# Kernel optimization log

Hardware: AMD Instinct MI355X
Metric: run time of the kernel (lower is better)

Reference implementation:

```python
import jax, jax.numpy as jnp
import numpy as np

B, S, F, H, C, L = 256, 128, 128, 512, 64, 16


def setup_inputs() -> dict:
    key = jax.random.key(0)
    ks = jax.random.split(key, 16)
    stdv = 1.0 / np.sqrt(H)
    u = lambda k, shape, s=stdv: jax.random.uniform(k, shape, jnp.float32, -s, s)
    W_ih = u(ks[0], (F, 4 * H))
    b_ih = u(ks[1], (4 * H,)).at[H:2 * H].set(1.0)  # forget-gate bias init = 1
    W_hh = u(ks[2], (H, 4 * H))
    b_hh = u(ks[3], (4 * H,)).at[H:2 * H].set(1.0)
    cg_w1 = u(ks[4], (C, H))
    cg_b1 = u(ks[5], (H,))
    cg_w2 = u(ks[6], (H, 3 * H))
    cg_b2 = jnp.ones((3 * H,), jnp.float32)  # context_gate[-2].bias.fill_(1.0)
    mu_w = u(ks[7], (H, L))
    mu_b = u(ks[8], (L,))
    lv_w = u(ks[9], (H, L))
    lv_b = u(ks[10], (L,))
    dec_w1 = u(ks[11], (L, H))
    dec_b1 = u(ks[12], (H,))
    dec_w2 = u(ks[13], (H, F))
    dec_b2 = u(ks[14], (F,))
    kx, kc, ke = jax.random.split(ks[15], 3)
    return dict(
        x=jax.random.normal(kx, (B, S, F), jnp.float32),
        context=jax.random.normal(kc, (B, C), jnp.float32),
        eps=jax.random.normal(ke, (B, L), jnp.float32),
        W_ih=W_ih, b_ih=b_ih, W_hh=W_hh, b_hh=b_hh,
        cg_w1=cg_w1, cg_b1=cg_b1, cg_w2=cg_w2, cg_b2=cg_b2,
        mu_w=mu_w, mu_b=mu_b, lv_w=lv_w, lv_b=lv_b,
        dec_w1=dec_w1, dec_b1=dec_b1, dec_w2=dec_w2, dec_b2=dec_b2,
    )


def reference(x, context, eps, W_ih, b_ih, W_hh, b_hh, cg_w1, cg_b1, cg_w2, cg_b2,
              mu_w, mu_b, lv_w, lv_b, dec_w1, dec_b1, dec_w2, dec_b2):
    Bsz, Slen, _ = x.shape
    Hd = W_hh.shape[0]
    # context is static across time -> context-gate computed once (same math as
    # recomputing identically at each step)
    ctx = jax.nn.sigmoid(jax.nn.relu(context @ cg_w1 + cg_b1) @ cg_w2 + cg_b2)  # [B, 3H]
    ci, cf, co = jnp.split(ctx, 3, axis=1)
    # precompute input projections for all timesteps: [S, B, 4H]
    xg = jnp.einsum('bsf,fk->sbk', x, W_ih) + b_ih

    def step(carry, xg_t):
        h, c = carry
        gates = xg_t + h @ W_hh + b_hh
        i, f, g, o = jnp.split(gates, 4, axis=1)
        i = jax.nn.sigmoid(i) * ci
        f = jax.nn.sigmoid(f) * cf
        g = jnp.tanh(g)
        o = jax.nn.sigmoid(o) * co
        c_next = f * c + i * g
        h_next = o * jnp.tanh(c_next)
        return (h_next, c_next), None

    h0 = jnp.zeros((Bsz, Hd), x.dtype)
    (h, _), _ = jax.lax.scan(step, (h0, h0), xg)

    mu = h @ mu_w + mu_b
    log_var = h @ lv_w + lv_b
    z = mu + eps * jnp.exp(0.5 * log_var)  # reparameterize
    recon_x = jax.nn.relu(z @ dec_w1 + dec_b1) @ dec_w2 + dec_b2
    return recon_x, mu, log_var
```

## Files before the change

### kernel.cpp

```cpp
#include <hip/hip_runtime.h>
#include <cstdint>
#include <cstddef>

#define B_ 256
#define S_ 128
#define F_ 128
#define H_ 512
#define C_ 64
#define L_ 16

typedef __attribute__((ext_vector_type(8))) short short8;
typedef __attribute__((ext_vector_type(4))) float f4;
typedef __attribute__((ext_vector_type(4))) unsigned int u4;

__device__ __forceinline__ unsigned short f2bf(float f) {
  union { float f; unsigned u; } v; v.f = f;
  unsigned r = v.u + 0x7fffu + ((v.u >> 16) & 1u);
  return (unsigned short)(r >> 16);
}
__device__ __forceinline__ float sigmoid_(float x) { return 1.0f / (1.0f + __expf(-x)); }
__device__ __forceinline__ float tanh_(float x) {
  x = fminf(15.f, fmaxf(-15.f, x));
  float e = __expf(2.f * x);
  return (e - 1.f) / (e + 1.f);
}

__global__ void fused_pre(const float* __restrict__ W_hh, const float* __restrict__ W_ih,
                          const float* __restrict__ b_ih, const float* __restrict__ b_hh,
                          const float* __restrict__ x, const float* __restrict__ context,
                          const float* __restrict__ cg_w1, const float* __restrict__ cg_b1,
                          unsigned short* __restrict__ Wpk, unsigned short* __restrict__ Wipk,
                          float* __restrict__ bc, unsigned short* __restrict__ xfr,
                          float* __restrict__ hid1) {
  int bid = blockIdx.x;
  if (bid < 648) {
    int t = bid * blockDim.x + threadIdx.x;
    if (t < 131072) {
      int lane = t & 63, r = t >> 6;
      int kit = r & 15, z = r >> 4;
      int gate = z & 3, w = (z >> 2) & 3, g = z >> 4;
      int col = gate * 512 + g * 64 + w * 16 + (lane & 15);
      int k0 = kit * 32 + ((lane >> 4) << 3);
#pragma unroll
      for (int j = 0; j < 8; j++)
        Wpk[t * 8 + j] = f2bf(W_hh[(k0 + j) * 2048 + col]);
    } else if (t < 131072 + 32768) {
      int t2 = t - 131072;
      int lane = t2 & 63, r = t2 >> 6;
      int kit = r & 3, z = r >> 2;
      int gate = z & 3, w = (z >> 2) & 3, g = z >> 4;
      int col = gate * 512 + g * 64 + w * 16 + (lane & 15);
      int k0 = kit * 32 + ((lane >> 4) << 3);
#pragma unroll
      for (int j = 0; j < 8; j++)
        Wipk[t2 * 8 + j] = f2bf(W_ih[(k0 + j) * 2048 + col]);
    } else if (t < 131072 + 32768 + 2048) {
      int i = t - 131072 - 32768;
      bc[i] = b_ih[i] + b_hh[i];
    }
  } else if (bid < 2696) {
    int o8 = (bid - 648) * blockDim.x + threadIdx.x;
    int m = o8 & 15, kb = (o8 >> 4) & 15, Rg = (o8 >> 8) & 15, s = o8 >> 12;
    int b = Rg * 16 + m;
    const float* src = x + (b * S_ + s) * F_ + kb * 8;
    unsigned short* dst = xfr + o8 * 8;
#pragma unroll
    for (int j = 0; j < 8; j++) dst[j] = f2bf(src[j]);
  } else {
    __shared__ float cc[C_];
    int b = bid - 2696, t = threadIdx.x;
    if (t < C_) cc[t] = context[b * C_ + t];
    __syncthreads();
    for (int j = t; j < H_; j += 256) {
      float acc = cg_b1[j];
#pragma unroll 8
      for (int k = 0; k < C_; k++) acc = fmaf(cc[k], cg_w1[k * H_ + j], acc);
      hid1[b * H_ + j] = fmaxf(acc, 0.f);
    }
  }
}

__global__ void ctx2_kernel(const float* __restrict__ hid1, const float* __restrict__ w2,
                            const float* __restrict__ b2, float* __restrict__ ctxg) {
  __shared__ float hr[4 * H_];
  int r0 = blockIdx.x * 4, t = threadIdx.x;
  for (int i = t; i < 4 * H_; i += 256) hr[i] = hid1[r0 * H_ + i];
  __syncthreads();
  float acc[4][6];
#pragma unroll
  for (int r = 0; r < 4; r++)
#pragma unroll
    for (int i = 0; i < 6; i++) acc[r][i] = 0.f;
  for (int k = 0; k < H_; k++) {
    float w[6];
#pragma unroll
    for (int i = 0; i < 6; i++) w[i] = w2[k * 1536 + t + i * 256];
#pragma unroll
    for (int r = 0; r < 4; r++) {
      float hv = hr[r * H_ + k];
#pragma unroll
      for (int i = 0; i < 6; i++) acc[r][i] = fmaf(hv, w[i], acc[r][i]);
    }
  }
#pragma unroll
  for (int r = 0; r < 4; r++)
#pragma unroll
    for (int i = 0; i < 6; i++) {
      int col = t + i * 256;
      ctxg[(r0 + r) * 1536 + col] = sigmoid_(acc[r][i] + b2[col]);
    }
}

__global__ void __launch_bounds__(256, 1) lstm_kernel(
    const unsigned short* __restrict__ xfr, const unsigned short* __restrict__ Wpk,
    const unsigned short* __restrict__ Wipk, const float* __restrict__ bc,
    const float* __restrict__ ctxg, float* __restrict__ hfinal,
    unsigned int* __restrict__ hb0, unsigned int* __restrict__ hb1) {
  __shared__ __align__(16) unsigned short lds_h[8192];

  int tid = threadIdx.x, lane = tid & 63, wid = tid >> 6;
  int bt = blockIdx.x >> 3, g = blockIdx.x & 7;

  short8 wf[4][16], wfi[4][4];
#pragma unroll
  for (int gate = 0; gate < 4; gate++) {
    const short8* wp = (const short8*)Wpk + (size_t)((g * 16 + wid * 4 + gate) * 16) * 64 + lane;
#pragma unroll
    for (int kit = 0; kit < 16; kit++) wf[gate][kit] = wp[kit * 64];
    const short8* wip = (const short8*)Wipk + (size_t)((g * 16 + wid * 4 + gate) * 4) * 64 + lane;
#pragma unroll
    for (int kit = 0; kit < 4; kit++) wfi[gate][kit] = wip[kit * 64];
  }

  int q = lane >> 4, n = lane & 15;
  int colglob = g * 64 + wid * 16 + n;
  float ci_[4], cf_[4], co_[4], cst[4] = {0.f, 0.f, 0.f, 0.f};
#pragma unroll
  for (int r = 0; r < 4; r++) {
    int brow = bt * 16 + q * 4 + r;
    ci_[r] = ctxg[brow * 1536 + colglob];
    cf_[r] = ctxg[brow * 1536 + 512 + colglob];
    co_[r] = ctxg[brow * 1536 + 1024 + colglob];
  }
  float bi = bc[colglob], bff = bc[512 + colglob], bgg = bc[1024 + colglob], bo = bc[1536 + colglob];

  int hsub = (bt * 16 + (colglob >> 5)) * 512 + ((colglob >> 3) & 3) * 128 + (colglob & 7);

  for (int t = 0; t < S_; t++) {
    const unsigned int* hread = (t & 1) ? hb1 : hb0;
    unsigned int* hwrite = (t & 1) ? hb0 : hb1;
    unsigned tt = (unsigned)t;
    unsigned tt1 = (unsigned)(t + 1);

    u4 xt[4];
#pragma unroll
    for (int kit = 0; kit < 4; kit++)
      xt[kit] = *(const u4*)(xfr + ((size_t)(t * 16 + bt) * 4 + kit) * 512 + lane * 8);

    u4 a0, a1, a2, a3, a4, a5, a6, a7;
    {
      const unsigned int* base = hread + (bt * 16 + wid * 4) * 512 + lane * 8;
      const unsigned int* p0 = base;
      const unsigned int* p1 = base + 4;
      const unsigned int* p2 = base + 512;
      const unsigned int* p3 = base + 516;
      const unsigned int* p4 = base + 1024;
      const unsigned int* p5 = base + 1028;
      const unsigned int* p6 = base + 1536;
      const unsigned int* p7 = base + 1540;
      for (;;) {
        asm volatile(
            "global_load_dwordx4 %0, %8, off sc0 sc1\n\t"
            "global_load_dwordx4 %1, %9, off sc0 sc1\n\t"
            "global_load_dwordx4 %2, %10, off sc0 sc1\n\t"
            "global_load_dwordx4 %3, %11, off sc0 sc1\n\t"
            "global_load_dwordx4 %4, %12, off sc0 sc1\n\t"
            "global_load_dwordx4 %5, %13, off sc0 sc1\n\t"
            "global_load_dwordx4 %6, %14, off sc0 sc1\n\t"
            "global_load_dwordx4 %7, %15, off sc0 sc1\n\t"
            "s_waitcnt vmcnt(0)"
            : "=&v"(a0), "=&v"(a1), "=&v"(a2), "=&v"(a3),
              "=&v"(a4), "=&v"(a5), "=&v"(a6), "=&v"(a7)
            : "v"(p0), "v"(p1), "v"(p2), "v"(p3),
              "v"(p4), "v"(p5), "v"(p6), "v"(p7)
            : "memory");
        unsigned bad = 0;
#pragma unroll
        for (int c = 0; c < 4; c++) {
          bad |= (a0[c] >> 16) ^ tt; bad |= (a1[c] >> 16) ^ tt;
          bad |= (a2[c] >> 16) ^ tt; bad |= (a3[c] >> 16) ^ tt;
          bad |= (a4[c] >> 16) ^ tt; bad |= (a5[c] >> 16) ^ tt;
          bad |= (a6[c] >> 16) ^ tt; bad |= (a7[c] >> 16) ^ tt;
        }
        if (__all(bad == 0)) break;
      }
    }

    {
      u4 P;
      P.x = (a0[0] & 0xffffu) | (a0[1] << 16);
      P.y = (a0[2] & 0xffffu) | (a0[3] << 16);
      P.z = (a1[0] & 0xffffu) | (a1[1] << 16);
      P.w = (a1[2] & 0xffffu) | (a1[3] << 16);
      *(u4*)(lds_h + (wid * 4 + 0) * 512 + lane * 8) = P;
      P.x = (a2[0] & 0xffffu) | (a2[1] << 16);
      P.y = (a2[2] & 0xffffu) | (a2[3] << 16);
      P.z = (a3[0] & 0xffffu) | (a3[1] << 16);
      P.w = (a3[2] & 0xffffu) | (a3[3] << 16);
      *(u4*)(lds_h + (wid * 4 + 1) * 512 + lane * 8) = P;
      P.x = (a4[0] & 0xffffu) | (a4[1] << 16);
      P.y = (a4[2] & 0xffffu) | (a4[3] << 16);
      P.z = (a5[0] & 0xffffu) | (a5[1] << 16);
      P.w = (a5[2] & 0xffffu) | (a5[3] << 16);
      *(u4*)(lds_h + (wid * 4 + 2) * 512 + lane * 8) = P;
      P.x = (a6[0] & 0xffffu) | (a6[1] << 16);
      P.y = (a6[2] & 0xffffu) | (a6[3] << 16);
      P.z = (a7[0] & 0xffffu) | (a7[1] << 16);
      P.w = (a7[2] & 0xffffu) | (a7[3] << 16);
      *(u4*)(lds_h + (wid * 4 + 3) * 512 + lane * 8) = P;
    }
    __syncthreads();

    f4 acc[4];
#pragma unroll
    for (int gate = 0; gate < 4; gate++) acc[gate] = (f4){0.f, 0.f, 0.f, 0.f};
#pragma unroll
    for (int kit = 0; kit < 4; kit++) {
      short8 a = __builtin_bit_cast(short8, xt[kit]);
#pragma unroll
      for (int gate = 0; gate < 4; gate++)
        acc[gate] = __builtin_amdgcn_mfma_f32_16x16x32_bf16(a, wfi[gate][kit], acc[gate], 0, 0, 0);
    }

#pragma unroll
    for (int kit = 0; kit < 16; kit++) {
      short8 a = *(const short8*)(lds_h + kit * 512 + lane * 8);
#pragma unroll
      for (int gate = 0; gate < 4; gate++)
        acc[gate] = __builtin_amdgcn_mfma_f32_16x16x32_bf16(a, wf[gate][kit], acc[gate], 0, 0, 0);
    }

    float hv[4];
#pragma unroll
    for (int r = 0; r < 4; r++) {
      float gi = acc[0][r] + bi, gf = acc[1][r] + bff, gc = acc[2][r] + bgg, go = acc[3][r] + bo;
      float iv = ci_[r] * sigmoid_(gi);
      float fv = cf_[r] * sigmoid_(gf);
      float ov = co_[r] * sigmoid_(go);
      float gv = tanh_(gc);
      float c = fv * cst[r] + iv * gv;
      cst[r] = c;
      hv[r] = ov * tanh_(c);
    }

#pragma unroll
    for (int r = 0; r < 4; r++) {
      unsigned int* d = hwrite + hsub + (q * 4 + r) * 8;
      unsigned val = (tt1 << 16) | (unsigned)f2bf(hv[r]);
      asm volatile("global_store_dword %0, %1, off sc0 sc1" :: "v"(d), "v"(val) : "memory");
    }
    if (t == S_ - 1) {
#pragma unroll
      for (int r = 0; r < 4; r++)
        hfinal[(bt * 16 + q * 4 + r) * H_ + colglob] = hv[r];
    }
    __syncthreads();
  }
}

__global__ void post_kernel(const float* __restrict__ hfinal, const float* __restrict__ eps,
                            const float* __restrict__ mu_w, const float* __restrict__ mu_b,
                            const float* __restrict__ lv_w, const float* __restrict__ lv_b,
                            const float* __restrict__ dw1, const float* __restrict__ db1,
                            const float* __restrict__ dw2, const float* __restrict__ db2,
                            float* __restrict__ out) {
  __shared__ float sh[H_], sh1[H_], smu[L_], slv[L_], sz[L_];
  int b = blockIdx.x, t = threadIdx.x;
  for (int i = t; i < H_; i += 256) sh[i] = hfinal[b * H_ + i];
  __syncthreads();
  {
    int o = t >> 3, sub = t & 7, l = o & 15;
    const float* w = (o < 16) ? mu_w : lv_w;
    float acc = 0.f;
    int k0 = sub * 64;
#pragma unroll 8
    for (int k = k0; k < k0 + 64; k++) acc = fmaf(sh[k], w[k * L_ + l], acc);
#pragma unroll
    for (int d = 4; d >= 1; d >>= 1) acc += __shfl_down(acc, d, 8);
    if (sub == 0) {
      if (o < 16) { float v = acc + mu_b[l]; smu[l] = v; out[32768 + b * 16 + l] = v; }
      else        { float v = acc + lv_b[l]; slv[l] = v; out[36864 + b * 16 + l] = v; }
    }
  }
  __syncthreads();
  if (t < L_) sz[t] = smu[t] + eps[b * L_ + t] * __expf(0.5f * slv[t]);
  __syncthreads();
  for (int j = t; j < H_; j += 256) {
    float acc = db1[j];
#pragma unroll
    for (int l = 0; l < L_; l++) acc = fmaf(sz[l], dw1[l * H_ + j], acc);
    sh1[j] = fmaxf(acc, 0.f);
  }
  __syncthreads();
  if (t < F_) {
    float acc = db2[t];
    for (int k = 0; k < H_; k++) acc = fmaf(sh1[k], dw2[k * F_ + t], acc);
    out[b * F_ + t] = acc;
  }
}

extern "C" void kernel_launch(void* const* d_in, const int* in_sizes, int n_in,
                              void* d_out, int out_size, void* d_ws, size_t ws_size,
                              hipStream_t stream) {
  const float* x      = (const float*)d_in[0];
  const float* ctxin  = (const float*)d_in[1];
  const float* eps    = (const float*)d_in[2];
  const float* W_ih   = (const float*)d_in[3];
  const float* b_ih   = (const float*)d_in[4];
  const float* W_hh   = (const float*)d_in[5];
  const float* b_hh   = (const float*)d_in[6];
  const float* cg_w1  = (const float*)d_in[7];
  const float* cg_b1  = (const float*)d_in[8];
  const float* cg_w2  = (const float*)d_in[9];
  const float* cg_b2  = (const float*)d_in[10];
  const float* mu_w   = (const float*)d_in[11];
  const float* mu_b   = (const float*)d_in[12];
  const float* lv_w   = (const float*)d_in[13];
  const float* lv_b   = (const float*)d_in[14];
  const float* dec_w1 = (const float*)d_in[15];
  const float* dec_b1 = (const float*)d_in[16];
  const float* dec_w2 = (const float*)d_in[17];
  const float* dec_b2 = (const float*)d_in[18];
  float* out = (float*)d_out;

  char* ws = (char*)d_ws;
  size_t off = 0;
  auto alloc = [&](size_t bytes) { char* p = ws + off; off = (off + bytes + 255) & ~(size_t)255; return p; };

  unsigned int* hb0 = (unsigned int*)alloc((size_t)B_ * H_ * 4);
  unsigned int* hb1 = (unsigned int*)alloc((size_t)B_ * H_ * 4);
  size_t zero_bytes = off;
  unsigned short* xfr  = (unsigned short*)alloc((size_t)B_ * S_ * F_ * 2);
  unsigned short* Wpk  = (unsigned short*)alloc((size_t)H_ * 2048 * 2);
  unsigned short* Wipk = (unsigned short*)alloc((size_t)F_ * 2048 * 2);
  float* bc    = (float*)alloc(2048 * 4);
  float* ctxg  = (float*)alloc((size_t)B_ * 1536 * 4);
  float* hid1  = (float*)alloc((size_t)B_ * H_ * 4);
  float* hfin  = (float*)alloc((size_t)B_ * H_ * 4);
  (void)ws_size; (void)in_sizes; (void)n_in; (void)out_size;

  hipMemsetAsync(d_ws, 0, zero_bytes, stream);

  fused_pre<<<2952, 256, 0, stream>>>(W_hh, W_ih, b_ih, b_hh, x, ctxin, cg_w1, cg_b1,
                                      Wpk, Wipk, bc, xfr, hid1);
  ctx2_kernel<<<64, 256, 0, stream>>>(hid1, cg_w2, cg_b2, ctxg);
  lstm_kernel<<<128, 256, 0, stream>>>(xfr, Wpk, Wipk, bc, ctxg, hfin, hb0, hb1);
  post_kernel<<<256, 256, 0, stream>>>(hfin, eps, mu_w, mu_b, lv_w, lv_b,
                                       dec_w1, dec_b1, dec_w2, dec_b2, out);
}
```

Baseline: 650.4 us.

## Double-buffer LDS hidden state, drop trailing barrier, selectively re-poll stale loads

The LDS buffer holding the hidden state becomes double-buffered per timestep, which lets the trailing __syncthreads at the end of each step be removed. The spin-wait on the cross-block hidden-state flags now reloads only the chunks that are still stale, with an s_sleep between polls, instead of reissuing all eight loads. Sigmoid and tanh use the hardware reciprocal instead of a full-precision division, while the context-gate sigmoid keeps exact division. Together these target per-step synchronisation and polling overhead in the sequential recurrence, at the cost of slightly lower activation precision and possible added latency from the sleep.

```diff
diff --git a/kernel.cpp b/kernel.cpp
--- a/kernel.cpp
+++ b/kernel.cpp
@@ -18,11 +18,13 @@
   unsigned r = v.u + 0x7fffu + ((v.u >> 16) & 1u);
   return (unsigned short)(r >> 16);
 }
-__device__ __forceinline__ float sigmoid_(float x) { return 1.0f / (1.0f + __expf(-x)); }
+__device__ __forceinline__ float sigmoid_(float x) {
+  return __builtin_amdgcn_rcpf(1.0f + __expf(-x));
+}
 __device__ __forceinline__ float tanh_(float x) {
   x = fminf(15.f, fmaxf(-15.f, x));
   float e = __expf(2.f * x);
-  return (e - 1.f) / (e + 1.f);
+  return (e - 1.f) * __builtin_amdgcn_rcpf(e + 1.f);
 }
 
 __global__ void fused_pre(const float* __restrict__ W_hh, const float* __restrict__ W_ih,
@@ -107,7 +109,7 @@
 #pragma unroll
     for (int i = 0; i < 6; i++) {
       int col = t + i * 256;
-      ctxg[(r0 + r) * 1536 + col] = sigmoid_(acc[r][i] + b2[col]);
+      ctxg[(r0 + r) * 1536 + col] = 1.0f / (1.0f + __expf(-(acc[r][i] + b2[col])));
     }
 }
 
@@ -116,7 +118,7 @@
     const unsigned short* __restrict__ Wipk, const float* __restrict__ bc,
     const float* __restrict__ ctxg, float* __restrict__ hfinal,
     unsigned int* __restrict__ hb0, unsigned int* __restrict__ hb1) {
-  __shared__ __align__(16) unsigned short lds_h[8192];
+  __shared__ __align__(16) unsigned short lds_h[2][8192];
 
   int tid = threadIdx.x, lane = tid & 63, wid = tid >> 6;
   int bt = blockIdx.x >> 3, g = blockIdx.x & 7;
@@ -149,6 +151,7 @@
   for (int t = 0; t < S_; t++) {
     const unsigned int* hread = (t & 1) ? hb1 : hb0;
     unsigned int* hwrite = (t & 1) ? hb0 : hb1;
+    int cur = t & 1;
     unsigned tt = (unsigned)t;
     unsigned tt1 = (unsigned)(t + 1);
 
@@ -168,56 +171,108 @@
       const unsigned int* p5 = base + 1028;
       const unsigned int* p6 = base + 1536;
       const unsigned int* p7 = base + 1540;
-      for (;;) {
+      asm volatile(
+          "global_load_dwordx4 %0, %8, off sc0 sc1\n\t"
+          "global_load_dwordx4 %1, %9, off sc0 sc1\n\t"
+          "global_load_dwordx4 %2, %10, off sc0 sc1\n\t"
+          "global_load_dwordx4 %3, %11, off sc0 sc1\n\t"
+          "global_load_dwordx4 %4, %12, off sc0 sc1\n\t"
+          "global_load_dwordx4 %5, %13, off sc0 sc1\n\t"
+          "global_load_dwordx4 %6, %14, off sc0 sc1\n\t"
+          "global_load_dwordx4 %7, %15, off sc0 sc1\n\t"
+          "s_waitcnt vmcnt(0)"
+          : "=&v"(a0), "=&v"(a1), "=&v"(a2), "=&v"(a3),
+            "=&v"(a4), "=&v"(a5), "=&v"(a6), "=&v"(a7)
+          : "v"(p0), "v"(p1), "v"(p2), "v"(p3),
+            "v"(p4), "v"(p5), "v"(p6), "v"(p7)
+          : "memory");
+      auto bad = [&](const u4& a) -> unsigned {
+        return ((a[0] >> 16) ^ tt) | ((a[1] >> 16) ^ tt)
+             | ((a[2] >> 16) ^ tt) | ((a[3] >> 16) ^ tt);
+      };
+      unsigned m = (__any((int)(bad(a0) != 0)) ? 1u : 0u)
+                 | (__any((int)(bad(a1) != 0)) ? 2u : 0u)
+                 | (__any((int)(bad(a2) != 0)) ? 4u : 0u)
+                 | (__any((int)(bad(a3) != 0)) ? 8u : 0u)
+                 | (__any((int)(bad(a4) != 0)) ? 16u : 0u)
+                 | (__any((int)(bad(a5) != 0)) ? 32u : 0u)
+                 | (__any((int)(bad(a6) != 0)) ? 64u : 0u)
+                 | (__any((int)(bad(a7) != 0)) ? 128u : 0u);
+      while (m) {
+        __builtin_amdgcn_s_sleep(2);
         asm volatile(
-            "global_load_dwordx4 %0, %8, off sc0 sc1\n\t"
-            "global_load_dwordx4 %1, %9, off sc0 sc1\n\t"
-            "global_load_dwordx4 %2, %10, off sc0 sc1\n\t"
-            "global_load_dwordx4 %3, %11, off sc0 sc1\n\t"
-            "global_load_dwordx4 %4, %12, off sc0 sc1\n\t"
-            "global_load_dwordx4 %5, %13, off sc0 sc1\n\t"
-            "global_load_dwordx4 %6, %14, off sc0 sc1\n\t"
-            "global_load_dwordx4 %7, %15, off sc0 sc1\n\t"
+            "s_bitcmp1_b32 %16, 0\n\t"
+            "s_cbranch_scc0 Lp0_%=\n\t"
+            "global_load_dwordx4 %0, %8, off sc0 sc1\n"
+            "Lp0_%=:\n\t"
+            "s_bitcmp1_b32 %16, 1\n\t"
+            "s_cbranch_scc0 Lp1_%=\n\t"
+            "global_load_dwordx4 %1, %9, off sc0 sc1\n"
+            "Lp1_%=:\n\t"
+            "s_bitcmp1_b32 %16, 2\n\t"
+            "s_cbranch_scc0 Lp2_%=\n\t"
+            "global_load_dwordx4 %2, %10, off sc0 sc1\n"
+            "Lp2_%=:\n\t"
+            "s_bitcmp1_b32 %16, 3\n\t"
+            "s_cbranch_scc0 Lp3_%=\n\t"
+            "global_load_dwordx4 %3, %11, off sc0 sc1\n"
+            "Lp3_%=:\n\t"
+            "s_bitcmp1_b32 %16, 4\n\t"
+            "s_cbranch_scc0 Lp4_%=\n\t"
+            "global_load_dwordx4 %4, %12, off sc0 sc1\n"
+            "Lp4_%=:\n\t"
+            "s_bitcmp1_b32 %16, 5\n\t"
+            "s_cbranch_scc0 Lp5_%=\n\t"
+            "global_load_dwordx4 %5, %13, off sc0 sc1\n"
+            "Lp5_%=:\n\t"
+            "s_bitcmp1_b32 %16, 6\n\t"
+            "s_cbranch_scc0 Lp6_%=\n\t"
+            "global_load_dwordx4 %6, %14, off sc0 sc1\n"
+            "Lp6_%=:\n\t"
+            "s_bitcmp1_b32 %16, 7\n\t"
+            "s_cbranch_scc0 Lp7_%=\n\t"
+            "global_load_dwordx4 %7, %15, off sc0 sc1\n"
+            "Lp7_%=:\n\t"
             "s_waitcnt vmcnt(0)"
-            : "=&v"(a0), "=&v"(a1), "=&v"(a2), "=&v"(a3),
-              "=&v"(a4), "=&v"(a5), "=&v"(a6), "=&v"(a7)
+            : "+v"(a0), "+v"(a1), "+v"(a2), "+v"(a3),
+              "+v"(a4), "+v"(a5), "+v"(a6), "+v"(a7)
             : "v"(p0), "v"(p1), "v"(p2), "v"(p3),
-              "v"(p4), "v"(p5), "v"(p6), "v"(p7)
-            : "memory");
-        unsigned bad = 0;
-#pragma unroll
-        for (int c = 0; c < 4; c++) {
-          bad |= (a0[c] >> 16) ^ tt; bad |= (a1[c] >> 16) ^ tt;
-          bad |= (a2[c] >> 16) ^ tt; bad |= (a3[c] >> 16) ^ tt;
-          bad |= (a4[c] >> 16) ^ tt; bad |= (a5[c] >> 16) ^ tt;
-          bad |= (a6[c] >> 16) ^ tt; bad |= (a7[c] >> 16) ^ tt;
-        }
-        if (__all(bad == 0)) break;
+              "v"(p4), "v"(p5), "v"(p6), "v"(p7), "s"(m)
+            : "memory", "scc");
+        m = (__any((int)(bad(a0) != 0)) ? 1u : 0u)
+          | (__any((int)(bad(a1) != 0)) ? 2u : 0u)
+          | (__any((int)(bad(a2) != 0)) ? 4u : 0u)
+          | (__any((int)(bad(a3) != 0)) ? 8u : 0u)
+          | (__any((int)(bad(a4) != 0)) ? 16u : 0u)
+          | (__any((int)(bad(a5) != 0)) ? 32u : 0u)
+          | (__any((int)(bad(a6) != 0)) ? 64u : 0u)
+          | (__any((int)(bad(a7) != 0)) ? 128u : 0u);
       }
     }
 
     {
+      unsigned short* lh = &lds_h[cur][0];
       u4 P;
       P.x = (a0[0] & 0xffffu) | (a0[1] << 16);
       P.y = (a0[2] & 0xffffu) | (a0[3] << 16);
       P.z = (a1[0] & 0xffffu) | (a1[1] << 16);
       P.w = (a1[2] & 0xffffu) | (a1[3] << 16);
-      *(u4*)(lds_h + (wid * 4 + 0) * 512 + lane * 8) = P;
+      *(u4*)(lh + (wid * 4 + 0) * 512 + lane * 8) = P;
       P.x = (a2[0] & 0xffffu) | (a2[1] << 16);
       P.y = (a2[2] & 0xffffu) | (a2[3] << 16);
       P.z = (a3[0] & 0xffffu) | (a3[1] << 16);
       P.w = (a3[2] & 0xffffu) | (a3[3] << 16);
-      *(u4*)(lds_h + (wid * 4 + 1) * 512 + lane * 8) = P;
+      *(u4*)(lh + (wid * 4 + 1) * 512 + lane * 8) = P;
       P.x = (a4[0] & 0xffffu) | (a4[1] << 16);
       P.y = (a4[2] & 0xffffu) | (a4[3] << 16);
       P.z = (a5[0] & 0xffffu) | (a5[1] << 16);
       P.w = (a5[2] & 0xffffu) | (a5[3] << 16);
-      *(u4*)(lds_h + (wid * 4 + 2) * 512 + lane * 8) = P;
+      *(u4*)(lh + (wid * 4 + 2) * 512 + lane * 8) = P;
       P.x = (a6[0] & 0xffffu) | (a6[1] << 16);
       P.y = (a6[2] & 0xffffu) | (a6[3] << 16);
       P.z = (a7[0] & 0xffffu) | (a7[1] << 16);
       P.w = (a7[2] & 0xffffu) | (a7[3] << 16);
-      *(u4*)(lds_h + (wid * 4 + 3) * 512 + lane * 8) = P;
+      *(u4*)(lh + (wid * 4 + 3) * 512 + lane * 8) = P;
     }
     __syncthreads();
 
@@ -234,7 +289,7 @@
 
 #pragma unroll
     for (int kit = 0; kit < 16; kit++) {
-      short8 a = *(const short8*)(lds_h + kit * 512 + lane * 8);
+      short8 a = *(const short8*)(&lds_h[cur][0] + kit * 512 + lane * 8);
 #pragma unroll
       for (int gate = 0; gate < 4; gate++)
         acc[gate] = __builtin_amdgcn_mfma_f32_16x16x32_bf16(a, wf[gate][kit], acc[gate], 0, 0, 0);
@@ -264,7 +319,6 @@
       for (int r = 0; r < 4; r++)
         hfinal[(bt * 16 + q * 4 + r) * H_ + colglob] = hv[r];
     }
-    __syncthreads();
   }
 }
 
```

Result: faster. 624.2 us (-4.0%).
